# Optimization experiments

Measured on AMD Instinct MI355X. Metric: run time of the kernel, lower is better.

Reference implementation:

```python
import jax, jax.numpy as jnp
import numpy as np

N_ATOMS = 50000
N_EDGES = 1600000
N_CONF = 2000
N_MOL = 500
H = 128          # hidden_channels
F = 128          # num_filters
G = 50           # num_gaussians
L = 6            # num_interactions
CUTOFF = 5.0
LOG2 = np.float32(np.log(2.0))


def ssp(x):
    # ShiftedSoftplus: softplus(x) - log(2)
    return jax.nn.softplus(x) - LOG2


def setup_inputs() -> dict:
    key = jax.random.key(0)
    ks = jax.random.split(key, 16)
    s = 1.0 / np.sqrt(H)
    inp = {
        "z": jax.random.randint(ks[0], (N_ATOMS,), 0, 120),
        "pos": jax.random.normal(ks[1], (N_ATOMS, 3), jnp.float32) * 2.0,
        "edge_index": jax.random.randint(ks[2], (2, N_EDGES), 0, N_ATOMS),
        "atom_to_conf": jnp.sort(jax.random.randint(ks[3], (N_ATOMS,), 0, N_CONF)),
        "conf_to_mol": jnp.sort(jax.random.randint(ks[4], (N_CONF,), 0, N_MOL)),
        "emb": jax.random.normal(ks[5], (120, H), jnp.float32),
        "iw1": jax.random.normal(ks[6], (L, G, F), jnp.float32) / np.sqrt(G),
        "ib1": jnp.zeros((L, F), jnp.float32),
        "iw2": jax.random.normal(ks[7], (L, F, F), jnp.float32) * s,
        "ib2": jnp.zeros((L, F), jnp.float32),
        "il1": jax.random.normal(ks[8], (L, H, F), jnp.float32) * s,
        "il2w": jax.random.normal(ks[9], (L, F, H), jnp.float32) * s,
        "il2b": jnp.zeros((L, H), jnp.float32),
        "ilw": jax.random.normal(ks[10], (L, H, H), jnp.float32) * s,
        "ilb": jnp.zeros((L, H), jnp.float32),
        "l1w": jax.random.normal(ks[11], (H, H), jnp.float32) * s,
        "l1b": jnp.zeros((H,), jnp.float32),
        "l2w": jax.random.normal(ks[12], (H, H), jnp.float32) * s,
        "l2b": jnp.zeros((H,), jnp.float32),
        "h1w": jax.random.normal(ks[13], (H, H // 2), jnp.float32) * s,
        "h1b": jnp.zeros((H // 2,), jnp.float32),
        "h2w": jax.random.normal(ks[14], (H // 2, 1), jnp.float32) / np.sqrt(H // 2),
        "h2b": jnp.zeros((1,), jnp.float32),
    }
    return inp


def reference(pos, emb, iw1, ib1, iw2, ib2, il1, il2w, il2b, ilw, ilb,
              l1w, l1b, l2w, l2b, h1w, h1b, h2w, h2b,
              z, edge_index, atom_to_conf, conf_to_mol):
    src = edge_index[0]
    dst = edge_index[1]

    # edge weights (distances), eps guards grad at coincident points
    diff = pos[src] - pos[dst]                     # (E,3)
    d = jnp.sqrt(jnp.sum(diff * diff, axis=-1) + 1e-12)  # (E,)

    # Gaussian smearing of distances
    offset = jnp.linspace(0.0, CUTOFF, G, dtype=jnp.float32)
    coeff = -0.5 / (offset[1] - offset[0]) ** 2
    edge_attr = jnp.exp(coeff * (d[:, None] - offset) ** 2)   # (E,G)

    # cosine cutoff
    C = 0.5 * (jnp.cos(d * (jnp.pi / CUTOFF)) + 1.0)          # (E,)

    h = emb[z]                                                 # (N,H)
    for k in range(L):
        # filter MLP on edge attributes
        W = ssp(edge_attr @ iw1[k] + ib1[k]) @ iw2[k] + ib2[k]  # (E,F)
        W = W * C[:, None]
        x = h @ il1[k]                                          # (N,F)
        msg = x[src] * W                                        # (E,F)
        agg = jax.ops.segment_sum(msg, dst, num_segments=N_ATOMS)  # (N,F)
        x = agg @ il2w[k] + il2b[k]
        x = ssp(x)
        x = x @ ilw[k] + ilb[k]
        h = h + x

    h = ssp(h @ l1w + l1b) @ l2w + l2b                          # (N,H)

    conf = jax.ops.segment_sum(h, atom_to_conf, num_segments=N_CONF)   # (C,H)
    mol = jax.ops.segment_sum(conf, conf_to_mol, num_segments=N_MOL)   # (M,H)

    pred = (ssp(mol @ h1w + h1b) @ h2w + h2b)[:, 0]             # (M,)
    return pred
```

## Files before the change

### kernel.cpp

```cpp
#include <hip/hip_runtime.h>
#include <math.h>

namespace {

constexpr int NA  = 50000;
constexpr int NE  = 1600000;
constexpr int NM  = 500;
constexpr int H   = 128;
constexpr int G   = 50;
constexpr int L   = 6;
constexpr int TBL = 8192;
constexpr int TSTR = (TBL + 1) * H;
constexpr int PAD = 80;
constexpr float DMAX = 5.6f;
constexpr int SB  = 64;
constexpr int SCH = (NA + SB - 1) / SB;

typedef _Float16 half8 __attribute__((ext_vector_type(8)));
typedef float f32x4 __attribute__((ext_vector_type(4)));
struct hpair { _Float16 x, y; };

__device__ __forceinline__ float sspf(float v) {
    return fmaxf(v, 0.0f) + log1pf(expf(-fabsf(v))) - 0.6931471805599453f;
}
__device__ __forceinline__ unsigned short f2h(float f) {
    _Float16 h = (_Float16)f;
    return __builtin_bit_cast(unsigned short, h);
}
__device__ __forceinline__ half8 cvt8(float4 a, float4 b) {
    half8 r;
    r[0] = (_Float16)a.x; r[1] = (_Float16)a.y; r[2] = (_Float16)a.z; r[3] = (_Float16)a.w;
    r[4] = (_Float16)b.x; r[5] = (_Float16)b.y; r[6] = (_Float16)b.z; r[7] = (_Float16)b.w;
    return r;
}
__device__ __forceinline__ float hlo(unsigned v) {
    return (float)__builtin_bit_cast(hpair, v).x;
}
__device__ __forceinline__ float hhi(unsigned v) {
    return (float)__builtin_bit_cast(hpair, v).y;
}
__device__ __forceinline__ int bofs(int nrow, int g) {
    int gs = (g & 8) | ((g ^ nrow) & 7);
    return nrow * 128 + gs * 8;
}
__device__ __forceinline__ int tofs(int row, int g) {
    int gs = (g & 8) | ((g ^ row) & 7);
    return (row << 7) + (gs << 3);
}


__global__ void edge_build(const float* __restrict__ pos, const int* __restrict__ ei,
                           int* __restrict__ counts, unsigned* __restrict__ meta) {
    int e = blockIdx.x * 256 + threadIdx.x;
    if (e >= NE) return;
    int s = ei[e], t = ei[NE + e];
    float dx = pos[3*s]   - pos[3*t];
    float dy = pos[3*s+1] - pos[3*t+1];
    float dz = pos[3*s+2] - pos[3*t+2];
    float d = sqrtf(dx*dx + dy*dy + dz*dz + 1e-12f);
    float u = d * ((float)(TBL - 1) / DMAX);
    if (u < (float)(TBL - 1)) {
        int idx = (int)(u + 0.5f);
        int r = atomicAdd(&counts[t], 1);
        if (r < PAD) meta[(size_t)t * PAD + r] = (unsigned)s | ((unsigned)idx << 16);
    }
}

__global__ void meta_pad(const int* __restrict__ deg, unsigned* __restrict__ meta) {
    int i = blockIdx.x * 256 + threadIdx.x;
    if (i >= NA) return;
    int n = min(deg[i], PAD);
    int n8 = (n + 7) & ~7;
    const unsigned pv = (unsigned)TBL << 16;
    for (int r = n; r < n8; ++r) meta[(size_t)i * PAD + r] = pv;
}


__global__ __launch_bounds__(256) void sort_hist(const int* __restrict__ deg,
                                                 int* __restrict__ part) {
    __shared__ int bins[PAD + 1];
    int b = blockIdx.x, tid = threadIdx.x;
    if (tid <= PAD) bins[tid] = 0;
    __syncthreads();
    int i0 = b * SCH, i1 = min(i0 + SCH, NA);
    for (int i = i0 + tid; i < i1; i += 256)
        atomicAdd(&bins[min(deg[i], PAD)], 1);
    __syncthreads();
    if (tid <= PAD) part[b * (PAD + 1) + tid] = bins[tid];
}

__global__ __launch_bounds__(128) void sort_scan(int* __restrict__ part) {
    __shared__ int totals[PAD + 1];
    int b = threadIdx.x;
    if (b <= PAD) {
        int s = 0;
        for (int k = 0; k < SB; ++k) s += part[k * (PAD + 1) + b];
        totals[b] = s;
    }
    __syncthreads();
    if (b == 0) {
        int acc = 0;
        for (int v = 0; v <= PAD; ++v) { int c = totals[v]; totals[v] = acc; acc += c; }
    }
    __syncthreads();
    if (b <= PAD) {
        int acc = totals[b];
        for (int k = 0; k < SB; ++k) {
            int c = part[k * (PAD + 1) + b];
            part[k * (PAD + 1) + b] = acc;
            acc += c;
        }
    }
}

__global__ __launch_bounds__(256) void sort_scatter(const int* __restrict__ deg,
                                                    const int* __restrict__ part,
                                                    int* __restrict__ order) {
    __shared__ int cur[PAD + 1];
    int b = blockIdx.x, tid = threadIdx.x;
    if (tid <= PAD) cur[tid] = part[b * (PAD + 1) + tid];
    __syncthreads();
    int i0 = b * SCH, i1 = min(i0 + SCH, NA);
    for (int i = i0 + tid; i < i1; i += 256) {
        int p = atomicAdd(&cur[min(deg[i], PAD)], 1);
        order[p] = i;
    }
}


__global__ void prep_weights(const float* __restrict__ il1, const float* __restrict__ il2w,
                             const float* __restrict__ ilw, const float* __restrict__ iw2,
                             const float* __restrict__ l1w, const float* __restrict__ l2w,
                             const float* __restrict__ iw1,
                             unsigned short* __restrict__ il1t, unsigned short* __restrict__ il2wt,
                             unsigned short* __restrict__ ilwt, unsigned short* __restrict__ iw2t,
                             unsigned short* __restrict__ l1wt, unsigned short* __restrict__ l2wt,
                             unsigned short* __restrict__ iw1t) {
    int m = blockIdx.y;
    int e = blockIdx.x * 256 + threadIdx.x;
    if (m < 26) {
        const float* src; unsigned short* dst;
        if (m < 6)       { src = il1  + (size_t)m * 16384;        dst = il1t  + (size_t)m * 16384; }
        else if (m < 12) { src = il2w + (size_t)(m - 6) * 16384;  dst = il2wt + (size_t)(m - 6) * 16384; }
        else if (m < 18) { src = ilw  + (size_t)(m - 12) * 16384; dst = ilwt  + (size_t)(m - 12) * 16384; }
        else if (m < 24) { src = iw2  + (size_t)(m - 18) * 16384; dst = iw2t  + (size_t)(m - 18) * 16384; }
        else if (m == 24){ src = l1w; dst = l1wt; }
        else             { src = l2w; dst = l2wt; }
        int n = e >> 7, k = e & 127;
        dst[e] = f2h(src[k * 128 + n]);
    } else {
        int l = m - 26;
        if (e < 8192) {
            int n = e >> 6, k = e & 63;
            float v = (k < G) ? iw1[(size_t)l * G * H + k * H + n] : 0.0f;
            iw1t[(size_t)l * 8192 + e] = f2h(v);
        }
    }
}


__global__ __launch_bounds__(256) void table_gemm(const unsigned short* __restrict__ iw1t,
                                                  const float* __restrict__ ib1,
                                                  const unsigned short* __restrict__ iw2t,
                                                  const float* __restrict__ ib2,
                                                  unsigned short* __restrict__ wtab) {
    __shared__ unsigned short Bs[16384];
    __shared__ _Float16 Ts[64 * 136];
    int l = blockIdx.y;
    int tid = threadIdx.x;
    int w = tid >> 6, lane = tid & 63, lr = lane & 15, lq = lane >> 4;
    int r0 = blockIdx.x * 64;
    int trow = w * 16;
    const float step  = DMAX / (float)(TBL - 1);
    const float sp    = 5.0f / 49.0f;
    const float coeff = -0.5f / (sp * sp);

    if (blockIdx.x == 0 && tid < H)
        wtab[(size_t)l * TSTR + (size_t)TBL * H + tid] = 0;

    for (int i = tid; i < 1024; i += 256) {
        int row = i >> 3, g = i & 7;
        int gs = (g ^ row) & 7;
        *(uint4*)&Bs[row * 64 + gs * 8] = *(const uint4*)&iw1t[(size_t)l * 8192 + i * 8];
    }
    for (int i = tid; i < 64 * 64; i += 256) {
        int r = i >> 6, g = i & 63;
        float d = (float)(r0 + r) * step;
        float dd = d - (float)g * sp;
        Ts[r * 136 + g] = (_Float16)((g < G) ? expf(coeff * dd * dd) : 0.0f);
    }
    float Cj[4];
    #pragma unroll
    for (int j = 0; j < 4; ++j) {
        float d = (float)(r0 + trow + 4 * lq + j) * step;
        Cj[j] = 0.5f * (cosf(d * (3.14159265358979323846f / 5.0f)) + 1.0f);
    }
    __syncthreads();
    half8 af[2];
    #pragma unroll
    for (int ks = 0; ks < 2; ++ks)
        af[ks] = *(const half8*)&Ts[(trow + lr) * 136 + ks * 32 + lq * 8];
    __syncthreads();

    #pragma unroll
    for (int n = 0; n < 8; ++n) {
        f32x4 acc = {0.f, 0.f, 0.f, 0.f};
        #pragma unroll
        for (int ks = 0; ks < 2; ++ks) {
            int row = n * 16 + lr, g = ks * 4 + lq;
            half8 bf = *(const half8*)&Bs[row * 64 + ((g ^ row) & 7) * 8];
            acc = __builtin_amdgcn_mfma_f32_16x16x32_f16(af[ks], bf, acc, 0, 0, 0);
        }
        float b = ib1[l * H + n * 16 + lr];
        #pragma unroll
        for (int j = 0; j < 4; ++j)
            Ts[(trow + 4 * lq + j) * 136 + n * 16 + lr] = (_Float16)sspf(acc[j] + b);
    }
    __syncthreads();
    for (int i = tid; i < 2048; i += 256) {
        int row = i >> 4, g = i & 15;
        *(uint4*)&Bs[bofs(row, g)] = *(const uint4*)&iw2t[(size_t)l * 16384 + i * 8];
    }
    half8 tf[4];
    #pragma unroll
    for (int ks = 0; ks < 4; ++ks)
        tf[ks] = *(const half8*)&Ts[(trow + lr) * 136 + ks * 32 + lq * 8];
    __syncthreads();
    #pragma unroll
    for (int n = 0; n < 8; ++n) {
        f32x4 acc = {0.f, 0.f, 0.f, 0.f};
        #pragma unroll
        for (int ks = 0; ks < 4; ++ks) {
            half8 bf = *(const half8*)&Bs[bofs(n * 16 + lr, ks * 4 + lq)];
            acc = __builtin_amdgcn_mfma_f32_16x16x32_f16(tf[ks], bf, acc, 0, 0, 0);
        }
        float b = ib2[l * H + n * 16 + lr];
        #pragma unroll
        for (int j = 0; j < 4; ++j) {
            int row = r0 + trow + 4 * lq + j;
            wtab[(size_t)l * TSTR + (size_t)row * H + n * 16 + lr] =
                f2h((acc[j] + b) * Cj[j]);
        }
    }
}


__global__ __launch_bounds__(256) void gemm_hx(const int* __restrict__ z,
                                               const float* __restrict__ emb,
                                               const unsigned short* __restrict__ Bt,
                                               unsigned short* __restrict__ hout,
                                               unsigned short* __restrict__ xout, int M) {
    __shared__ unsigned short Bs[16384];
    int tid = threadIdx.x;
    int w = tid >> 6, lane = tid & 63, lr = lane & 15, lq = lane >> 4;
    int r0 = blockIdx.x * 64 + w * 16;
    for (int i = tid; i < 2048; i += 256) {
        int row = i >> 4, g = i & 15;
        *(uint4*)&Bs[bofs(row, g)] = *(const uint4*)&Bt[i * 8];
    }
    int row = min(r0 + lr, M - 1);
    const float* arow = emb + (size_t)z[row] * H;
    half8 af[4];
    #pragma unroll
    for (int ks = 0; ks < 4; ++ks) {
        float4 a = *(const float4*)(arow + ks * 32 + lq * 8);
        float4 b = *(const float4*)(arow + ks * 32 + lq * 8 + 4);
        af[ks] = cvt8(a, b);
        if (r0 + lr < M)
            *(half8*)&hout[(size_t)(r0 + lr) * H + ks * 32 + lq * 8] = af[ks];
    }
    __syncthreads();
    #pragma unroll
    for (int n = 0; n < 8; ++n) {
        f32x4 acc = {0.f, 0.f, 0.f, 0.f};
        #pragma unroll
        for (int ks = 0; ks < 4; ++ks) {
            half8 bf = *(const half8*)&Bs[bofs(n * 16 + lr, ks * 4 + lq)];
            acc = __builtin_amdgcn_mfma_f32_16x16x32_f16(af[ks], bf, acc, 0, 0, 0);
        }
        #pragma unroll
        for (int j = 0; j < 4; ++j) {
            int orow = r0 + 4 * lq + j;
            if (orow < M) xout[(size_t)orow * H + n * 16 + lr] = f2h(acc[j]);
        }
    }
}


template<int RES, int HASX, int OUT16>
__global__ __launch_bounds__(512, 4) void node_fused(const unsigned short* __restrict__ Ain16,
                                                     const float* __restrict__ bias1,
                                                     const unsigned short* __restrict__ B1t,
                                                     const unsigned short* __restrict__ hres16,
                                                     unsigned short* __restrict__ hout16,
                                                     float* __restrict__ houtf,
                                                     const float* __restrict__ bias2,
                                                     const unsigned short* __restrict__ B2t,
                                                     const unsigned short* __restrict__ B3t,
                                                     unsigned short* __restrict__ xout, int M) {
    __shared__ unsigned short Bs[16384];
    __shared__ _Float16 Ts[128 * 128];
    int tid = threadIdx.x;
    int w = tid >> 6, lane = tid & 63, lr = lane & 15, lq = lane >> 4;
    int r0 = blockIdx.x * 128 + w * 16;
    int trow = w * 16;

    for (int i = tid; i < 2048; i += 512) {
        int row = i >> 4, g = i & 15;
        *(uint4*)&Bs[bofs(row, g)] = *(const uint4*)&B1t[i * 8];
    }
    half8 af[4];
    {
        const unsigned short* arow = Ain16 + (size_t)min(r0 + lr, M - 1) * H;
        #pragma unroll
        for (int ks = 0; ks < 4; ++ks)
            af[ks] = *(const half8*)(arow + ks * 32 + lq * 8);
    }
    __syncthreads();

    #pragma unroll
    for (int n = 0; n < 8; ++n) {
        f32x4 acc = {0.f, 0.f, 0.f, 0.f};
        #pragma unroll
        for (int ks = 0; ks < 4; ++ks) {
            half8 bf = *(const half8*)&Bs[bofs(n * 16 + lr, ks * 4 + lq)];
            acc = __builtin_amdgcn_mfma_f32_16x16x32_f16(af[ks], bf, acc, 0, 0, 0);
        }
        float b = bias1[n * 16 + lr];
        int gran = (n * 16 + lr) >> 3, o = lr & 7;
        #pragma unroll
        for (int j = 0; j < 4; ++j)
            Ts[tofs(trow + 4 * lq + j, gran) + o] = (_Float16)sspf(acc[j] + b);
    }
    __syncthreads();
    for (int i = tid; i < 2048; i += 512) {
        int row = i >> 4, g = i & 15;
        *(uint4*)&Bs[bofs(row, g)] = *(const uint4*)&B2t[i * 8];
    }
    half8 tf[4];
    #pragma unroll
    for (int ks = 0; ks < 4; ++ks)
        tf[ks] = *(const half8*)&Ts[tofs(trow + lr, ks * 4 + lq)];
    __syncthreads();

    #pragma unroll
    for (int n = 0; n < 8; ++n) {
        f32x4 acc = {0.f, 0.f, 0.f, 0.f};
        #pragma unroll
        for (int ks = 0; ks < 4; ++ks) {
            half8 bf = *(const half8*)&Bs[bofs(n * 16 + lr, ks * 4 + lq)];
            acc = __builtin_amdgcn_mfma_f32_16x16x32_f16(tf[ks], bf, acc, 0, 0, 0);
        }
        float b = bias2[n * 16 + lr];
        int gran = (n * 16 + lr) >> 3, o = lr & 7;
        #pragma unroll
        for (int j = 0; j < 4; ++j) {
            int row = r0 + 4 * lq + j;
            float v = acc[j] + b;
            if (RES)
                v += (float)*(const _Float16*)&hres16[(size_t)min(row, M - 1) * H + n * 16 + lr];
            if (row < M) {
                if (OUT16) hout16[(size_t)row * H + n * 16 + lr] = f2h(v);
                else       houtf[(size_t)row * H + n * 16 + lr] = v;
            }
            if (HASX) Ts[tofs(trow + 4 * lq + j, gran) + o] = (_Float16)v;
        }
    }

    if (HASX) {
        __syncthreads();
        for (int i = tid; i < 2048; i += 512) {
            int row = i >> 4, g = i & 15;
            *(uint4*)&Bs[bofs(row, g)] = *(const uint4*)&B3t[i * 8];
        }
        half8 hf[4];
        #pragma unroll
        for (int ks = 0; ks < 4; ++ks)
            hf[ks] = *(const half8*)&Ts[tofs(trow + lr, ks * 4 + lq)];
        __syncthreads();
        #pragma unroll
        for (int n = 0; n < 8; ++n) {
            f32x4 acc = {0.f, 0.f, 0.f, 0.f};
            #pragma unroll
            for (int ks = 0; ks < 4; ++ks) {
                half8 bf = *(const half8*)&Bs[bofs(n * 16 + lr, ks * 4 + lq)];
                acc = __builtin_amdgcn_mfma_f32_16x16x32_f16(hf[ks], bf, acc, 0, 0, 0);
            }
            #pragma unroll
            for (int j = 0; j < 4; ++j) {
                int row = r0 + 4 * lq + j;
                if (row < M) xout[(size_t)row * H + n * 16 + lr] = f2h(acc[j]);
            }
        }
    }
}


__global__ __launch_bounds__(256) void edge_agg(const int* __restrict__ deg,
                                                const int* __restrict__ order,
                                                const unsigned* __restrict__ meta,
                                                const unsigned short* __restrict__ x,
                                                const unsigned short* __restrict__ wt,
                                                unsigned short* __restrict__ agg) {
    int wv = threadIdx.x >> 6, ln = threadIdx.x & 63;
    int a = ln >> 4, fl = ln & 15;
    int gw = (blockIdx.x << 2) + wv;
    int chunk = (gw % 250) * 50 + (gw / 250);
    int pos = (chunk << 2) + a;
    int i = order[pos];
    int n8 = (min(deg[i], PAD) + 7) & ~7;
    const unsigned* mrow = meta + (size_t)i * PAD;
    int f8 = fl << 3;
    float acc[8] = {};
    for (int p = 0; p < n8; p += 8) {
        unsigned mm[8];
        #pragma unroll
        for (int j = 0; j < 8; ++j) mm[j] = mrow[p + j];
        uint4 xv[8], wv8[8];
        #pragma unroll
        for (int j = 0; j < 8; ++j) {
            unsigned s = mm[j] & 0xFFFFu, idx = mm[j] >> 16;
            xv[j]  = *(const uint4*)(x  + ((size_t)s   << 7) + f8);
            wv8[j] = *(const uint4*)(wt + ((size_t)idx << 7) + f8);
        }
        #pragma unroll
        for (int j = 0; j < 8; ++j) {
            acc[0] += hlo(xv[j].x) * hlo(wv8[j].x);
            acc[1] += hhi(xv[j].x) * hhi(wv8[j].x);
            acc[2] += hlo(xv[j].y) * hlo(wv8[j].y);
            acc[3] += hhi(xv[j].y) * hhi(wv8[j].y);
            acc[4] += hlo(xv[j].z) * hlo(wv8[j].z);
            acc[5] += hhi(xv[j].z) * hhi(wv8[j].z);
            acc[6] += hlo(xv[j].w) * hlo(wv8[j].w);
            acc[7] += hhi(xv[j].w) * hhi(wv8[j].w);
        }
    }
    uint4 ov;
    ov.x = (unsigned)f2h(acc[0]) | ((unsigned)f2h(acc[1]) << 16);
    ov.y = (unsigned)f2h(acc[2]) | ((unsigned)f2h(acc[3]) << 16);
    ov.z = (unsigned)f2h(acc[4]) | ((unsigned)f2h(acc[5]) << 16);
    ov.w = (unsigned)f2h(acc[6]) | ((unsigned)f2h(acc[7]) << 16);
    *(uint4*)&agg[((size_t)i << 7) + f8] = ov;
}


__global__ void mol_bounds(const int* __restrict__ a2c, const int* __restrict__ c2m,
                           int* __restrict__ ms, int* __restrict__ me) {
    int i = blockIdx.x * 256 + threadIdx.x;
    if (i >= NA) return;
    int m = c2m[a2c[i]];
    int mp = (i == 0) ? -1 : c2m[a2c[i - 1]];
    if (m != mp) ms[m] = i;
    int mn = (i == NA - 1) ? -1 : c2m[a2c[i + 1]];
    if (m != mn) me[m] = i + 1;
}

__global__ __launch_bounds__(512) void mol_sum(const int* __restrict__ ms, const int* __restrict__ me,
                                               const float* __restrict__ h2buf, float* __restrict__ mol) {
    __shared__ float red[4][128];
    int m = blockIdx.x;
    int f = threadIdx.x & 127, q = threadIdx.x >> 7;
    float acc = 0.f;
    int e0 = ms[m], e1 = me[m];
    for (int i = e0 + q; i < e1; i += 4) acc += h2buf[((size_t)i << 7) + f];
    red[q][f] = acc;
    __syncthreads();
    if (q == 0) mol[(m << 7) + f] = red[0][f] + red[1][f] + red[2][f] + red[3][f];
}

__global__ void final_mlp(const float* __restrict__ mol, const float* __restrict__ h1w,
                          const float* __restrict__ h1b, const float* __restrict__ h2w,
                          const float* __restrict__ h2b, float* __restrict__ out) {
    int m = blockIdx.x;
    int j = threadIdx.x;
    float acc = h1b[j];
    for (int k = 0; k < H; ++k) acc += mol[(m << 7) + k] * h1w[k * 64 + j];
    float hv = sspf(acc) * h2w[j];
    #pragma unroll
    for (int off = 32; off > 0; off >>= 1) hv += __shfl_down(hv, off);
    if (j == 0) out[m] = hv + h2b[0];
}

}

extern "C" void kernel_launch(void* const* d_in, const int* in_sizes, int n_in,
                              void* d_out, int out_size, void* d_ws, size_t ws_size,
                              hipStream_t stream) {
    const int*   z    = (const int*)d_in[0];
    const float* pos  = (const float*)d_in[1];
    const int*   ei   = (const int*)d_in[2];
    const int*   a2c  = (const int*)d_in[3];
    const int*   c2m  = (const int*)d_in[4];
    const float* emb  = (const float*)d_in[5];
    const float* iw1  = (const float*)d_in[6];
    const float* ib1  = (const float*)d_in[7];
    const float* iw2  = (const float*)d_in[8];
    const float* ib2  = (const float*)d_in[9];
    const float* il1  = (const float*)d_in[10];
    const float* il2w = (const float*)d_in[11];
    const float* il2b = (const float*)d_in[12];
    const float* ilw  = (const float*)d_in[13];
    const float* ilb  = (const float*)d_in[14];
    const float* l1w  = (const float*)d_in[15];
    const float* l1b  = (const float*)d_in[16];
    const float* l2w  = (const float*)d_in[17];
    const float* l2b  = (const float*)d_in[18];
    const float* h1w  = (const float*)d_in[19];
    const float* h1b  = (const float*)d_in[20];
    const float* h2w  = (const float*)d_in[21];
    const float* h2b  = (const float*)d_in[22];
    float* out = (float*)d_out;
    (void)in_sizes; (void)n_in; (void)out_size; (void)ws_size;

    char* base = (char*)d_ws;
    size_t off = 0;
    auto carve = [&](size_t bytes) -> char* {
        char* p = base + off;
        off += (bytes + 255) & ~(size_t)255;
        return p;
    };
    unsigned short* hb    = (unsigned short*)carve((size_t)NA * H * 2);
    unsigned short* xb    = (unsigned short*)carve((size_t)NA * H * 2);
    float*          agg   = (float*)carve((size_t)NA * H * 4);
    unsigned short* wtab  = (unsigned short*)carve((size_t)L * TSTR * 2);
    unsigned*       meta  = (unsigned*)carve(((size_t)NA * PAD + 16) * 4);
    int*            counts= (int*)carve((size_t)NA * 4);
    int*            order = (int*)carve((size_t)NA * 4);
    int*            part  = (int*)carve((size_t)SB * (PAD + 1) * 4);
    int*            ms    = (int*)carve((size_t)NM * 4);
    int*            me    = (int*)carve((size_t)NM * 4);
    float*          mol   = (float*)carve((size_t)NM * H * 4);
    unsigned short* il1t  = (unsigned short*)carve((size_t)L * H * H * 2);
    unsigned short* il2wt = (unsigned short*)carve((size_t)L * H * H * 2);
    unsigned short* ilwt  = (unsigned short*)carve((size_t)L * H * H * 2);
    unsigned short* iw2t  = (unsigned short*)carve((size_t)L * H * H * 2);
    unsigned short* l1wt  = (unsigned short*)carve((size_t)H * H * 2);
    unsigned short* l2wt  = (unsigned short*)carve((size_t)H * H * 2);
    unsigned short* iw1t  = (unsigned short*)carve((size_t)L * H * 64 * 2);
    unsigned short* aggh  = (unsigned short*)agg;

    hipMemsetAsync(counts, 0, (size_t)NA * 4, stream);
    edge_build<<<NE / 256, 256, 0, stream>>>(pos, ei, counts, meta);
    meta_pad<<<(NA + 255) / 256, 256, 0, stream>>>(counts, meta);
    sort_hist<<<SB, 256, 0, stream>>>(counts, part);
    sort_scan<<<1, 128, 0, stream>>>(part);
    sort_scatter<<<SB, 256, 0, stream>>>(counts, part, order);

    prep_weights<<<dim3(64, 32), 256, 0, stream>>>(il1, il2w, ilw, iw2, l1w, l2w, iw1,
                                                   il1t, il2wt, ilwt, iw2t, l1wt, l2wt, iw1t);
    table_gemm<<<dim3(TBL / 64, L), 256, 0, stream>>>(iw1t, ib1, iw2t, ib2, wtab);

    const int NG  = (NA + 63) / 64;
    const int NGn = (NA + 127) / 128;
    gemm_hx<<<NG, 256, 0, stream>>>(z, emb, il1t, hb, xb, NA);
    for (int k = 0; k < L; ++k) {
        edge_agg<<<NA / 16, 256, 0, stream>>>(counts, order, meta, xb,
                                              wtab + (size_t)k * TSTR, aggh);
        if (k < L - 1) {
            node_fused<1, 1, 1><<<NGn, 512, 0, stream>>>(aggh,
                il2b + (size_t)k * H, il2wt + (size_t)k * H * H,
                hb, hb, nullptr, ilb + (size_t)k * H, ilwt + (size_t)k * H * H,
                il1t + (size_t)(k + 1) * H * H, xb, NA);
        } else {
            node_fused<1, 0, 1><<<NGn, 512, 0, stream>>>(aggh,
                il2b + (size_t)k * H, il2wt + (size_t)k * H * H,
                hb, hb, nullptr, ilb + (size_t)k * H, ilwt + (size_t)k * H * H,
                nullptr, nullptr, NA);
        }
    }
    node_fused<0, 0, 0><<<NGn, 512, 0, stream>>>(hb, l1b, l1wt, nullptr, nullptr, agg,
                                                 l2b, l2wt, nullptr, nullptr, NA);

    hipMemsetAsync(ms, 0, (size_t)NM * 4, stream);
    hipMemsetAsync(me, 0, (size_t)NM * 4, stream);
    mol_bounds<<<(NA + 255) / 256, 256, 0, stream>>>(a2c, c2m, ms, me);
    mol_sum<<<NM, 512, 0, stream>>>(ms, me, agg, mol);
    final_mlp<<<NM, 64, 0, stream>>>(mol, h1w, h1b, h2w, h2b, out);
}
```

Baseline: 741.1 us.

## Fuse final readout MLP into last interaction node kernel; replace meta padding with zeroed sentinel

The last interaction's node kernel now also runs the two readout GEMMs (l1w with shifted softplus, then l2w), keeping h in shared memory. This removes a separate kernel launch and a full round trip of h through global memory. Table row 0 becomes a zero sentinel: table indices are shifted by one and the meta array is memset to zero, so padded slots point at the zero row and the meta_pad kernel goes away. In exchange, a memset of the whole meta buffer is added, and the fused kernel carries extra register and shared-memory load plus more synchronisation.

Result: no change. 734.2 us (-0.9%).

```diff
diff --git a/kernel.cpp b/kernel.cpp
--- a/kernel.cpp
+++ b/kernel.cpp
@@ -60,19 +60,10 @@
     float d = sqrtf(dx*dx + dy*dy + dz*dz + 1e-12f);
     float u = d * ((float)(TBL - 1) / DMAX);
     if (u < (float)(TBL - 1)) {
-        int idx = (int)(u + 0.5f);
+        int idx = (int)(u + 0.5f) + 1;
         int r = atomicAdd(&counts[t], 1);
         if (r < PAD) meta[(size_t)t * PAD + r] = (unsigned)s | ((unsigned)idx << 16);
     }
-}
-
-__global__ void meta_pad(const int* __restrict__ deg, unsigned* __restrict__ meta) {
-    int i = blockIdx.x * 256 + threadIdx.x;
-    if (i >= NA) return;
-    int n = min(deg[i], PAD);
-    int n8 = (n + 7) & ~7;
-    const unsigned pv = (unsigned)TBL << 16;
-    for (int r = n; r < n8; ++r) meta[(size_t)i * PAD + r] = pv;
 }
 
 
@@ -176,7 +167,7 @@
     const float coeff = -0.5f / (sp * sp);
 
     if (blockIdx.x == 0 && tid < H)
-        wtab[(size_t)l * TSTR + (size_t)TBL * H + tid] = 0;
+        wtab[(size_t)l * TSTR + tid] = 0;
 
     for (int i = tid; i < 1024; i += 256) {
         int row = i >> 3, g = i & 7;
@@ -238,7 +229,7 @@
         #pragma unroll
         for (int j = 0; j < 4; ++j) {
             int row = r0 + trow + 4 * lq + j;
-            wtab[(size_t)l * TSTR + (size_t)row * H + n * 16 + lr] =
+            wtab[(size_t)l * TSTR + (size_t)(row + 1) * H + n * 16 + lr] =
                 f2h((acc[j] + b) * Cj[j]);
         }
     }
@@ -287,7 +278,7 @@
 }
 
 
-template<int RES, int HASX, int OUT16>
+template<int RES, int HASX, int FIN>
 __global__ __launch_bounds__(512, 4) void node_fused(const unsigned short* __restrict__ Ain16,
                                                      const float* __restrict__ bias1,
                                                      const unsigned short* __restrict__ B1t,
@@ -297,6 +288,9 @@
                                                      const float* __restrict__ bias2,
                                                      const unsigned short* __restrict__ B2t,
                                                      const unsigned short* __restrict__ B3t,
+                                                     const float* __restrict__ bias3,
+                                                     const unsigned short* __restrict__ B4t,
+                                                     const float* __restrict__ bias4,
                                                      unsigned short* __restrict__ xout, int M) {
     __shared__ unsigned short Bs[16384];
     __shared__ _Float16 Ts[128 * 128];
@@ -359,11 +353,8 @@
             float v = acc[j] + b;
             if (RES)
                 v += (float)*(const _Float16*)&hres16[(size_t)min(row, M - 1) * H + n * 16 + lr];
-            if (row < M) {
-                if (OUT16) hout16[(size_t)row * H + n * 16 + lr] = f2h(v);
-                else       houtf[(size_t)row * H + n * 16 + lr] = v;
-            }
-            if (HASX) Ts[tofs(trow + 4 * lq + j, gran) + o] = (_Float16)v;
+            if (!FIN && row < M) hout16[(size_t)row * H + n * 16 + lr] = f2h(v);
+            if (HASX || FIN) Ts[tofs(trow + 4 * lq + j, gran) + o] = (_Float16)v;
         }
     }
 
@@ -390,6 +381,58 @@
             for (int j = 0; j < 4; ++j) {
                 int row = r0 + 4 * lq + j;
                 if (row < M) xout[(size_t)row * H + n * 16 + lr] = f2h(acc[j]);
+            }
+        }
+    }
+
+    if (FIN) {
+        __syncthreads();
+        for (int i = tid; i < 2048; i += 512) {
+            int row = i >> 4, g = i & 15;
+            *(uint4*)&Bs[bofs(row, g)] = *(const uint4*)&B3t[i * 8];
+        }
+        half8 hf[4];
+        #pragma unroll
+        for (int ks = 0; ks < 4; ++ks)
+            hf[ks] = *(const half8*)&Ts[tofs(trow + lr, ks * 4 + lq)];
+        __syncthreads();
+        #pragma unroll
+        for (int n = 0; n < 8; ++n) {
+            f32x4 acc = {0.f, 0.f, 0.f, 0.f};
+            #pragma unroll
+            for (int ks = 0; ks < 4; ++ks) {
+                half8 bf = *(const half8*)&Bs[bofs(n * 16 + lr, ks * 4 + lq)];
+                acc = __builtin_amdgcn_mfma_f32_16x16x32_f16(hf[ks], bf, acc, 0, 0, 0);
+            }
+            float b = bias3[n * 16 + lr];
+            int gran = (n * 16 + lr) >> 3, o = lr & 7;
+            #pragma unroll
+            for (int j = 0; j < 4; ++j)
+                Ts[tofs(trow + 4 * lq + j, gran) + o] = (_Float16)sspf(acc[j] + b);
+        }
+        __syncthreads();
+        for (int i = tid; i < 2048; i += 512) {
+            int row = i >> 4, g = i & 15;
+            *(uint4*)&Bs[bofs(row, g)] = *(const uint4*)&B4t[i * 8];
+        }
+        half8 uf[4];
+        #pragma unroll
+        for (int ks = 0; ks < 4; ++ks)
+            uf[ks] = *(const half8*)&Ts[tofs(trow + lr, ks * 4 + lq)];
+        __syncthreads();
+        #pragma unroll
+        for (int n = 0; n < 8; ++n) {
+            f32x4 acc = {0.f, 0.f, 0.f, 0.f};
+            #pragma unroll
+            for (int ks = 0; ks < 4; ++ks) {
+                half8 bf = *(const half8*)&Bs[bofs(n * 16 + lr, ks * 4 + lq)];
+                acc = __builtin_amdgcn_mfma_f32_16x16x32_f16(uf[ks], bf, acc, 0, 0, 0);
+            }
+            float b = bias4[n * 16 + lr];
+            #pragma unroll
+            for (int j = 0; j < 4; ++j) {
+                int row = r0 + 4 * lq + j;
+                if (row < M) houtf[(size_t)row * H + n * 16 + lr] = acc[j] + b;
             }
         }
     }
@@ -540,8 +583,8 @@
     unsigned short* aggh  = (unsigned short*)agg;
 
     hipMemsetAsync(counts, 0, (size_t)NA * 4, stream);
+    hipMemsetAsync(meta, 0, ((size_t)NA * PAD + 16) * 4, stream);
     edge_build<<<NE / 256, 256, 0, stream>>>(pos, ei, counts, meta);
-    meta_pad<<<(NA + 255) / 256, 256, 0, stream>>>(counts, meta);
     sort_hist<<<SB, 256, 0, stream>>>(counts, part);
     sort_scan<<<1, 128, 0, stream>>>(part);
     sort_scatter<<<SB, 256, 0, stream>>>(counts, part, order);
@@ -557,19 +600,17 @@
         edge_agg<<<NA / 16, 256, 0, stream>>>(counts, order, meta, xb,
                                               wtab + (size_t)k * TSTR, aggh);
         if (k < L - 1) {
-            node_fused<1, 1, 1><<<NGn, 512, 0, stream>>>(aggh,
+            node_fused<1, 1, 0><<<NGn, 512, 0, stream>>>(aggh,
                 il2b + (size_t)k * H, il2wt + (size_t)k * H * H,
                 hb, hb, nullptr, ilb + (size_t)k * H, ilwt + (size_t)k * H * H,
-                il1t + (size_t)(k + 1) * H * H, xb, NA);
+                il1t + (size_t)(k + 1) * H * H, nullptr, nullptr, nullptr, xb, NA);
         } else {
             node_fused<1, 0, 1><<<NGn, 512, 0, stream>>>(aggh,
                 il2b + (size_t)k * H, il2wt + (size_t)k * H * H,
-                hb, hb, nullptr, ilb + (size_t)k * H, ilwt + (size_t)k * H * H,
-                nullptr, nullptr, NA);
-        }
-    }
-    node_fused<0, 0, 0><<<NGn, 512, 0, stream>>>(hb, l1b, l1wt, nullptr, nullptr, agg,
-                                                 l2b, l2wt, nullptr, nullptr, NA);
+                hb, nullptr, agg, ilb + (size_t)k * H, ilwt + (size_t)k * H * H,
+                l1wt, l1b, l2wt, l2b, nullptr, NA);
+        }
+    }
 
     hipMemsetAsync(ms, 0, (size_t)NM * 4, stream);
     hipMemsetAsync(me, 0, (size_t)NM * 4, stream);
```
